# Kernel tuning notes

Hardware: AMD Instinct MI355X
Metric: run time of the kernel (lower is better)

## Reference

```python
import jax, jax.numpy as jnp
import numpy as np

B, N, C = 32, 1000, 81
MAX_INST = 100
MIN_CONF = 0.7
NMS_THRESH = 0.3
WINDOW = (0.0, 0.0, 1.0, 1.0)  # normalized y1, x1, y2, x2


def _apply_deltas(boxes, deltas):
    # boxes, deltas: [N, 4] in (y1, x1, y2, x2) / (dy, dx, log_dh, log_dw)
    h = boxes[:, 2] - boxes[:, 0]
    w = boxes[:, 3] - boxes[:, 1]
    cy = boxes[:, 0] + 0.5 * h + deltas[:, 0] * h
    cx = boxes[:, 1] + 0.5 * w + deltas[:, 1] * w
    h = h * jnp.exp(deltas[:, 2])
    w = w * jnp.exp(deltas[:, 3])
    y1 = cy - 0.5 * h
    x1 = cx - 0.5 * w
    return jnp.stack([y1, x1, y1 + h, x1 + w], axis=1)


def _clip_boxes(boxes, window):
    wy1, wx1, wy2, wx2 = window
    return jnp.stack([
        jnp.clip(boxes[:, 0], wy1, wy2),
        jnp.clip(boxes[:, 1], wx1, wx2),
        jnp.clip(boxes[:, 2], wy1, wy2),
        jnp.clip(boxes[:, 3], wx1, wx2)], axis=1)


def _pairwise_iou(b):
    y1, x1, y2, x2 = b[:, 0], b[:, 1], b[:, 2], b[:, 3]
    area = (y2 - y1) * (x2 - x1)
    iy = jnp.maximum(jnp.minimum(y2[:, None], y2[None, :]) - jnp.maximum(y1[:, None], y1[None, :]), 0.0)
    ix = jnp.maximum(jnp.minimum(x2[:, None], x2[None, :]) - jnp.maximum(x1[:, None], x1[None, :]), 0.0)
    inter = iy * ix
    union = area[:, None] + area[None, :] - inter
    return inter / jnp.maximum(union, 1e-8)


def _refine_one(rois, probs, deltas, std_dev):
    n = rois.shape[0]
    class_ids = jnp.argmax(probs, axis=1)                 # [N]
    scores = jnp.max(probs, axis=1)                       # [N]
    # per-roi deltas for the predicted class, scaled by bbox_std_dev
    d = jnp.take_along_axis(deltas, class_ids[:, None, None], axis=1)[:, 0, :] * std_dev
    boxes = _clip_boxes(_apply_deltas(rois, d), WINDOW)   # [N, 4]
    valid = (class_ids > 0) & (scores >= MIN_CONF)        # drop background + low conf

    # sort by score descending (invalid at the end)
    order = jnp.argsort(-jnp.where(valid, scores, -jnp.inf))
    b = boxes[order]
    s = scores[order]
    c = class_ids[order]
    v = valid[order]

    # greedy per-class NMS on score-sorted boxes
    iou = _pairwise_iou(b)                                # [N, N]
    sup = (iou > NMS_THRESH) & (c[:, None] == c[None, :])
    idx = jnp.arange(n)

    def step(keep, i):
        row = sup[i] & (idx > i) & keep[i]
        return keep & ~row, None

    keep, _ = jax.lax.scan(step, v, jnp.arange(n))
    keep = jax.lax.stop_gradient(keep)

    # kept boxes are already score-ordered -> compact first MAX_INST into slots
    slot = jnp.where(keep, jnp.cumsum(keep) - 1, MAX_INST)
    slot = jnp.minimum(slot, MAX_INST)                    # overflow bucket
    rows = jnp.concatenate([b, c[:, None].astype(b.dtype), s[:, None]], axis=1)  # [N, 6]
    out = jnp.zeros((MAX_INST + 1, 6), b.dtype).at[slot].set(rows)[:MAX_INST]
    return out                                            # [MAX_INST, 6]


def setup_inputs() -> dict:
    key = jax.random.key(0)
    k1, k2, k3, k4, k5 = jax.random.split(key, 5)
    cy = jax.random.uniform(k1, (B, N))
    cx = jax.random.uniform(k2, (B, N))
    h = jax.random.uniform(k3, (B, N), minval=0.02, maxval=0.4)
    w = jax.random.uniform(k4, (B, N), minval=0.02, maxval=0.4)
    rois = jnp.stack([
        jnp.clip(cy - 0.5 * h, 0.0, 1.0),
        jnp.clip(cx - 0.5 * w, 0.0, 1.0),
        jnp.clip(cy + 0.5 * h, 0.0, 1.0),
        jnp.clip(cx + 0.5 * w, 0.0, 1.0)], axis=2).astype(jnp.float32)
    logits = jax.random.normal(k5, (B, N, C), dtype=jnp.float32) * 2.0
    mrcnn_class = jax.nn.softmax(logits, axis=-1)
    mrcnn_bbox = jax.random.normal(jax.random.fold_in(key, 7), (B, N, C, 4), dtype=jnp.float32)
    bbox_std_dev = jnp.array([0.1, 0.1, 0.2, 0.2], dtype=jnp.float32)
    return {"rois": rois, "mrcnn_class": mrcnn_class, "mrcnn_bbox": mrcnn_bbox, "bbox_std_dev": bbox_std_dev}


def reference(rois, mrcnn_class, mrcnn_bbox, bbox_std_dev):
    out = jax.vmap(lambda r, p, d: _refine_one(r, p, d, bbox_std_dev))(rois, mrcnn_class, mrcnn_bbox)
    return out.reshape(B, MAX_INST, 6)
```

## Files before the change

### kernel.cpp

```cpp
#include <hip/hip_runtime.h>
#include <math.h>

#define BB 32
#define NN 1000
#define CC 81
#define MAX_INST 100
#define MIN_CONF 0.7f
#define NMS_THRESH 0.3f
#define MCAP 1024
#define RCHUNK 192
#define WMAX 16

__global__ __launch_bounds__(256) void roi_kernel(
    const float* __restrict__ rois,
    const float* __restrict__ probs,
    const float* __restrict__ deltas,
    const float* __restrict__ std_dev,
    float* __restrict__ rec)
{
  int wg = blockIdx.x * 4 + (threadIdx.x >> 6);
  if (wg >= BB * NN) return;
  int lane = threadIdx.x & 63;

  const float* p = probs + (size_t)wg * CC;
  float v = p[lane];
  int   c = lane;
  if (lane + 64 < CC) {
    float v2 = p[lane + 64];
    if (v2 > v) { v = v2; c = lane + 64; }
  }
  for (int off = 32; off; off >>= 1) {
    float vo = __shfl_down(v, off);
    int   co = __shfl_down(c, off);
    if (vo > v || (vo == v && co < c)) { v = vo; c = co; }
  }

  if (lane == 0) {
    float4 dd = *(const float4*)(deltas + ((size_t)wg * CC + c) * 4);
    float4 r4 = *(const float4*)(rois + (size_t)wg * 4);
    float dy = dd.x * std_dev[0], dx = dd.y * std_dev[1];
    float dh = dd.z * std_dev[2], dw = dd.w * std_dev[3];
    float h = r4.z - r4.x, w = r4.w - r4.y;
    float cy = r4.x + 0.5f * h + dy * h;
    float cx = r4.y + 0.5f * w + dx * w;
    h *= expf(dh); w *= expf(dw);
    float y1 = cy - 0.5f * h, x1 = cx - 0.5f * w;
    float y2 = y1 + h,        x2 = x1 + w;
    y1 = fminf(fmaxf(y1, 0.f), 1.f); x1 = fminf(fmaxf(x1, 0.f), 1.f);
    y2 = fminf(fmaxf(y2, 0.f), 1.f); x2 = fminf(fmaxf(x2, 0.f), 1.f);
    float4* o = (float4*)(rec + (size_t)wg * 8);
    o[0] = make_float4(y1, x1, y2, x2);
    o[1] = make_float4(v, (float)c, 0.f, 0.f);
  }
}

__global__ __launch_bounds__(1024) void nms_kernel(
    const float* __restrict__ rec,
    float* __restrict__ out)
{
  const int b = blockIdx.x, t = threadIdx.x;

  __shared__ float cscore[MCAP];
  __shared__ int   cidx[MCAP];
  __shared__ float sy1[MCAP], sx1[MCAP], sy2[MCAP], sx2[MCAP];
  __shared__ int   scls[MCAP];
  __shared__ unsigned long long rows[RCHUNK][WMAX];
  __shared__ unsigned long long keepw[WMAX];
  __shared__ int cnt;

  for (int i = t; i < MAX_INST * 6; i += 1024)
    out[(size_t)b * MAX_INST * 6 + i] = 0.0f;
  if (t == 0) cnt = 0;
  __syncthreads();

  float y1 = 0, x1 = 0, y2 = 0, x2 = 0, score = 0;
  int cls = 0; bool valid = false; int pos = -1;
  if (t < NN) {
    const float4* rr = (const float4*)(rec + ((size_t)b * NN + t) * 8);
    float4 a = rr[0], s = rr[1];
    y1 = a.x; x1 = a.y; y2 = a.z; x2 = a.w;
    score = s.x; cls = (int)s.y;
    valid = (cls > 0) && (score >= MIN_CONF);
    if (valid) pos = atomicAdd(&cnt, 1);
  }
  if (valid) { cscore[pos] = score; cidx[pos] = t; }
  __syncthreads();
  const int M = cnt;
  const int W = (M + 63) >> 6;

  int r = 0;
  if (valid) {
    for (int j = 0; j < M; ++j) {
      float sj = cscore[j]; int ij = cidx[j];
      if (sj > score || (sj == score && ij < t)) ++r;
    }
    sy1[r] = y1; sx1[r] = x1; sy2[r] = y2; sx2[r] = x2; scls[r] = cls;
  }
  if (t < WMAX) {
    unsigned long long kw = 0ULL;
    int base = t * 64;
    if (base < M) {
      int nb = M - base;
      kw = (nb >= 64) ? ~0ULL : ((1ULL << nb) - 1ULL);
    }
    keepw[t] = kw;
  }
  __syncthreads();

  const int wv = t >> 6, lane = t & 63;
  for (int c0 = 0; c0 < M; c0 += RCHUNK) {
    int R = min(RCHUNK, M - c0);
    for (int task = wv; task < R * W; task += 16) {
      int i = c0 + task / W;
      int w = task % W;
      int j = w * 64 + lane;
      bool cond = false;
      float iy1 = sy1[i], ix1 = sx1[i], iy2 = sy2[i], ix2 = sx2[i];
      int ic = scls[i];
      if (j < M && j > i && scls[j] == ic) {
        float jy1 = sy1[j], jx1 = sx1[j], jy2 = sy2[j], jx2 = sx2[j];
        float ai = (iy2 - iy1) * (ix2 - ix1);
        float aj = (jy2 - jy1) * (jx2 - jx1);
        float iy = fmaxf(fminf(iy2, jy2) - fmaxf(iy1, jy1), 0.f);
        float ix = fmaxf(fminf(ix2, jx2) - fmaxf(ix1, jx1), 0.f);
        float inter = iy * ix;
        float uni = fmaxf(ai + aj - inter, 1e-8f);
        cond = (inter / uni) > NMS_THRESH;
      }
      unsigned long long word = __ballot(cond);
      if (lane == 0) rows[task / W][w] = word;
    }
    __syncthreads();
    if (t < 64) {
      unsigned long long kw = (t < W) ? keepw[t] : 0ULL;
      for (int i = c0; i < c0 + R; ++i) {
        unsigned long long kwi = __shfl((long long)kw, i >> 6);
        if ((((unsigned long long)kwi) >> (i & 63)) & 1ULL) {
          if (t < W) kw &= ~rows[i - c0][t];
        }
      }
      if (t < W) keepw[t] = kw;
    }
    __syncthreads();
  }

  if (valid) {
    unsigned long long kwme = keepw[r >> 6];
    if ((kwme >> (r & 63)) & 1ULL) {
      int slot = 0;
      for (int w = 0; w < (r >> 6); ++w) slot += __popcll(keepw[w]);
      slot += __popcll(kwme & ((1ULL << (r & 63)) - 1ULL));
      if (slot < MAX_INST) {
        float* o = out + ((size_t)b * MAX_INST + slot) * 6;
        o[0] = y1; o[1] = x1; o[2] = y2; o[3] = x2;
        o[4] = (float)cls; o[5] = score;
      }
    }
  }
}

extern "C" void kernel_launch(void* const* d_in, const int* in_sizes, int n_in,
                              void* d_out, int out_size, void* d_ws, size_t ws_size,
                              hipStream_t stream) {
  const float* rois    = (const float*)d_in[0];
  const float* probs   = (const float*)d_in[1];
  const float* deltas  = (const float*)d_in[2];
  const float* std_dev = (const float*)d_in[3];
  float* out = (float*)d_out;
  float* rec = (float*)d_ws;

  roi_kernel<<<(BB * NN + 3) / 4, 256, 0, stream>>>(rois, probs, deltas, std_dev, rec);
  nms_kernel<<<BB, 1024, 0, stream>>>(rec, out);
}
```

Before: 106.5 us.

## Compact valid ROIs in first kernel and shrink NMS block to 256 threads

The ROI kernel now filters out background and low-confidence ROIs and appends only valid ones to a per-image compacted list via global atomics, also zeroing the output. The NMS kernel reads just the compacted entries with a 256-thread block instead of scanning all 1000 records with 1024 threads. This cuts intermediate traffic and idle NMS threads, at the cost of an extra memset launch and atomic contention.

Measured after the change: 104.8 us, median of 2. Within noise of the previous version (-1.6%).

```diff
diff --git a/kernel.cpp b/kernel.cpp
--- a/kernel.cpp
+++ b/kernel.cpp
@@ -11,13 +11,22 @@
 #define RCHUNK 192
 #define WMAX 16
 
+
 __global__ __launch_bounds__(256) void roi_kernel(
     const float* __restrict__ rois,
     const float* __restrict__ probs,
     const float* __restrict__ deltas,
     const float* __restrict__ std_dev,
-    float* __restrict__ rec)
+    int* __restrict__ gcnt,
+    float* __restrict__ glist,
+    float* __restrict__ out)
 {
+  if (blockIdx.x == 0) {
+    float4* o4 = (float4*)out;
+    for (int i = threadIdx.x; i < BB * MAX_INST * 6 / 4; i += 256)
+      o4[i] = make_float4(0.f, 0.f, 0.f, 0.f);
+  }
+
   int wg = blockIdx.x * 4 + (threadIdx.x >> 6);
   if (wg >= BB * NN) return;
   int lane = threadIdx.x & 63;
@@ -35,7 +44,7 @@
     if (vo > v || (vo == v && co < c)) { v = vo; c = co; }
   }
 
-  if (lane == 0) {
+  if (lane == 0 && c > 0 && v >= MIN_CONF) {
     float4 dd = *(const float4*)(deltas + ((size_t)wg * CC + c) * 4);
     float4 r4 = *(const float4*)(rois + (size_t)wg * 4);
     float dy = dd.x * std_dev[0], dx = dd.y * std_dev[1];
@@ -48,14 +57,17 @@
     float y2 = y1 + h,        x2 = x1 + w;
     y1 = fminf(fmaxf(y1, 0.f), 1.f); x1 = fminf(fmaxf(x1, 0.f), 1.f);
     y2 = fminf(fmaxf(y2, 0.f), 1.f); x2 = fminf(fmaxf(x2, 0.f), 1.f);
-    float4* o = (float4*)(rec + (size_t)wg * 8);
+    int b = wg / NN, n = wg - b * NN;
+    int pos = atomicAdd(&gcnt[b], 1);
+    float4* o = (float4*)(glist + ((size_t)b * MCAP + pos) * 8);
     o[0] = make_float4(y1, x1, y2, x2);
-    o[1] = make_float4(v, (float)c, 0.f, 0.f);
+    o[1] = make_float4(v, (float)c, (float)n, 0.f);
   }
 }
 
-__global__ __launch_bounds__(1024) void nms_kernel(
-    const float* __restrict__ rec,
+__global__ __launch_bounds__(256) void nms_kernel(
+    const int* __restrict__ gcnt,
+    const float* __restrict__ glist,
     float* __restrict__ out)
 {
   const int b = blockIdx.x, t = threadIdx.x;
@@ -64,45 +76,36 @@
   __shared__ int   cidx[MCAP];
   __shared__ float sy1[MCAP], sx1[MCAP], sy2[MCAP], sx2[MCAP];
   __shared__ int   scls[MCAP];
+  __shared__ float sscr[MCAP];
   __shared__ unsigned long long rows[RCHUNK][WMAX];
   __shared__ unsigned long long keepw[WMAX];
-  __shared__ int cnt;
 
-  for (int i = t; i < MAX_INST * 6; i += 1024)
-    out[(size_t)b * MAX_INST * 6 + i] = 0.0f;
-  if (t == 0) cnt = 0;
+  const int M = gcnt[b];
+  const int W = (M + 63) >> 6;
+  const float* base = glist + (size_t)b * MCAP * 8;
+
+  for (int e = t; e < M; e += 256) {
+    const float4 s = ((const float4*)(base + (size_t)e * 8))[1];
+    cscore[e] = s.x; cidx[e] = (int)s.z;
+  }
   __syncthreads();
 
-  float y1 = 0, x1 = 0, y2 = 0, x2 = 0, score = 0;
-  int cls = 0; bool valid = false; int pos = -1;
-  if (t < NN) {
-    const float4* rr = (const float4*)(rec + ((size_t)b * NN + t) * 8);
-    float4 a = rr[0], s = rr[1];
-    y1 = a.x; x1 = a.y; y2 = a.z; x2 = a.w;
-    score = s.x; cls = (int)s.y;
-    valid = (cls > 0) && (score >= MIN_CONF);
-    if (valid) pos = atomicAdd(&cnt, 1);
-  }
-  if (valid) { cscore[pos] = score; cidx[pos] = t; }
-  __syncthreads();
-  const int M = cnt;
-  const int W = (M + 63) >> 6;
-
-  int r = 0;
-  if (valid) {
+  for (int e = t; e < M; e += 256) {
+    const float4 a = ((const float4*)(base + (size_t)e * 8))[0];
+    const float4 s = ((const float4*)(base + (size_t)e * 8))[1];
+    float sc = s.x; int oi = (int)s.z;
+    int r = 0;
     for (int j = 0; j < M; ++j) {
       float sj = cscore[j]; int ij = cidx[j];
-      if (sj > score || (sj == score && ij < t)) ++r;
+      if (sj > sc || (sj == sc && ij < oi)) ++r;
     }
-    sy1[r] = y1; sx1[r] = x1; sy2[r] = y2; sx2[r] = x2; scls[r] = cls;
+    sy1[r] = a.x; sx1[r] = a.y; sy2[r] = a.z; sx2[r] = a.w;
+    scls[r] = (int)s.y; sscr[r] = sc;
   }
   if (t < WMAX) {
     unsigned long long kw = 0ULL;
-    int base = t * 64;
-    if (base < M) {
-      int nb = M - base;
-      kw = (nb >= 64) ? ~0ULL : ((1ULL << nb) - 1ULL);
-    }
+    int nb = M - t * 64;
+    if (nb > 0) kw = (nb >= 64) ? ~0ULL : ((1ULL << nb) - 1ULL);
     keepw[t] = kw;
   }
   __syncthreads();
@@ -110,7 +113,7 @@
   const int wv = t >> 6, lane = t & 63;
   for (int c0 = 0; c0 < M; c0 += RCHUNK) {
     int R = min(RCHUNK, M - c0);
-    for (int task = wv; task < R * W; task += 16) {
+    for (int task = wv; task < R * W; task += 4) {
       int i = c0 + task / W;
       int w = task % W;
       int j = w * 64 + lane;
@@ -135,7 +138,7 @@
       unsigned long long kw = (t < W) ? keepw[t] : 0ULL;
       for (int i = c0; i < c0 + R; ++i) {
         unsigned long long kwi = __shfl((long long)kw, i >> 6);
-        if ((((unsigned long long)kwi) >> (i & 63)) & 1ULL) {
+        if ((kwi >> (i & 63)) & 1ULL) {
           if (t < W) kw &= ~rows[i - c0][t];
         }
       }
@@ -144,7 +147,7 @@
     __syncthreads();
   }
 
-  if (valid) {
+  for (int r = t; r < M; r += 256) {
     unsigned long long kwme = keepw[r >> 6];
     if ((kwme >> (r & 63)) & 1ULL) {
       int slot = 0;
@@ -152,8 +155,8 @@
       slot += __popcll(kwme & ((1ULL << (r & 63)) - 1ULL));
       if (slot < MAX_INST) {
         float* o = out + ((size_t)b * MAX_INST + slot) * 6;
-        o[0] = y1; o[1] = x1; o[2] = y2; o[3] = x2;
-        o[4] = (float)cls; o[5] = score;
+        o[0] = sy1[r]; o[1] = sx1[r]; o[2] = sy2[r]; o[3] = sx2[r];
+        o[4] = (float)scls[r]; o[5] = sscr[r];
       }
     }
   }
@@ -167,8 +170,12 @@
   const float* deltas  = (const float*)d_in[2];
   const float* std_dev = (const float*)d_in[3];
   float* out = (float*)d_out;
-  float* rec = (float*)d_ws;
 
-  roi_kernel<<<(BB * NN + 3) / 4, 256, 0, stream>>>(rois, probs, deltas, std_dev, rec);
-  nms_kernel<<<BB, 1024, 0, stream>>>(rec, out);
+  int*   gcnt  = (int*)d_ws;
+  float* glist = (float*)((char*)d_ws + 128);
+
+  hipMemsetAsync(gcnt, 0, 128, stream);
+  roi_kernel<<<(BB * NN + 3) / 4, 256, 0, stream>>>(rois, probs, deltas, std_dev,
+                                                    gcnt, glist, out);
+  nms_kernel<<<BB, 256, 0, stream>>>(gcnt, glist, out);
 }
```
